# Kernel tuning notes

Measured on AMD Instinct MI355X. Metric: run time of the kernel, lower is better.

Reference implementation:

```python
import jax, jax.numpy as jnp
import numpy as np
import math

MAX2D = 1001        # max_2d_position_embeddings
COORD = 128         # coordinate_size
SHAPE = 128         # shape_size
PE = 384            # pos_embed_size
HID = 768           # layout_hidden_size
PAD = 0             # pad_token_id
EPS = 1e-12
INIT = 1024         # sinusoidal init_size
BIG = 100000000


def sinusoidal_table(num_embeddings=INIT, dim=PE, padding_idx=PAD):
    half = dim // 2
    freq = np.exp(np.arange(half, dtype=np.float32) * (-math.log(10000.0) / (half - 1)))
    ang = np.arange(num_embeddings, dtype=np.float32)[:, None] * freq[None, :]
    tab = np.concatenate([np.sin(ang), np.cos(ang)], axis=1)
    if padding_idx is not None:
        tab[padding_idx, :] = 0.0
    return jnp.asarray(tab, dtype=jnp.float32)


def setup_inputs() -> dict:
    key = jax.random.key(0)
    ks = jax.random.split(key, 16)
    B, L = 2, 1024
    x1 = jax.random.randint(ks[0], (B, L), 0, 501, dtype=jnp.int32)
    y1 = jax.random.randint(ks[1], (B, L), 0, 501, dtype=jnp.int32)
    w = jax.random.randint(ks[2], (B, L), 0, 500, dtype=jnp.int32)
    h = jax.random.randint(ks[3], (B, L), 0, 500, dtype=jnp.int32)
    bbox = jnp.stack([x1, y1, x1 + w, y1 + h], axis=-1)  # [B,L,4], 0..1000
    attention_mask = jnp.ones((B, L), dtype=jnp.int32)
    s = 0.02
    inp = {
        'bbox': bbox,
        'attention_mask': attention_mask,
        'x_tab': jax.random.normal(ks[4], (MAX2D, COORD), jnp.float32) * s,
        'y_tab': jax.random.normal(ks[5], (MAX2D, COORD), jnp.float32) * s,
        'h_tab': jax.random.normal(ks[6], (MAX2D, SHAPE), jnp.float32) * s,
        'w_tab': jax.random.normal(ks[7], (MAX2D, SHAPE), jnp.float32) * s,
        'W_tl_w': jax.random.normal(ks[8], (HID, 2 * PE), jnp.float32) * s,
        'W_tl_b': jnp.zeros((HID,), jnp.float32),
        'W_tr_w': jax.random.normal(ks[9], (HID, 2 * PE), jnp.float32) * s,
        'W_tr_b': jnp.zeros((HID,), jnp.float32),
        'W_bl_w': jax.random.normal(ks[10], (HID, 2 * PE), jnp.float32) * s,
        'W_bl_b': jnp.zeros((HID,), jnp.float32),
        'W_br_w': jax.random.normal(ks[11], (HID, 2 * PE), jnp.float32) * s,
        'W_br_b': jnp.zeros((HID,), jnp.float32),
        'ln_g': jnp.ones((HID,), jnp.float32),
        'ln_b': jnp.zeros((HID,), jnp.float32),
        'params': 50,
    }
    return inp


def _knn_graph(bbox, mask, topk):
    # mask out padded boxes with a huge coordinate (matches masked_fill)
    bm = jnp.where((mask == 0)[..., None], BIG, bbox).astype(jnp.float32)
    xc = (bm[:, :, 0] + bm[:, :, 2]) / 2.0
    yc = (bm[:, :, 1] + bm[:, :, 3]) / 2.0
    dist = (xc[:, :, None] - xc[:, None, :]) ** 2 + (yc[:, :, None] - yc[:, None, :]) ** 2
    _, topk_index = jax.lax.top_k(-dist, topk)  # smallest distances
    topk_index = topk_index.astype(jnp.int32)
    B, L, _ = topk_index.shape
    lm = jnp.zeros((B, L, L), jnp.int32)
    b_ix = jnp.arange(B)[:, None, None]
    l_ix = jnp.arange(L)[None, :, None]
    lm = lm.at[b_ix, l_ix, topk_index].set(1)
    return topk_index, lm


def _rel_pos_emb(bbox, topk_index, sin_tab):
    # diff[b,i,k] = coord[b,i] - coord[b,topk_index[b,i,k]]
    gather = jax.vmap(lambda v, idx: v[idx])  # per-batch gather

    def diffs(c):
        d = c[:, :, None] - gather(c, topk_index)
        d = jnp.clip(d, 1 - MAX2D, MAX2D - 1)
        # torch negative indexing into the table wraps: idx % INIT
        return sin_tab[jnp.mod(d, INIT)]  # [B,L,K,PE]

    ex1 = diffs(bbox[:, :, 0])
    ey1 = diffs(bbox[:, :, 1])
    ex2 = diffs(bbox[:, :, 2])
    ey2 = diffs(bbox[:, :, 3])
    return ex1, ey1, ex2, ey2


def _linear(x, w, b):
    return jnp.einsum('blki,oi->blko', x, w) + b


def reference(bbox, attention_mask, x_tab, y_tab, h_tab, w_tab,
              W_tl_w, W_tl_b, W_tr_w, W_tr_b, W_bl_w, W_bl_b, W_br_w, W_br_b,
              ln_g, ln_b, params):
    sin_tab = sinusoidal_table()
    # spatial position embeddings
    layout_emb = jnp.concatenate([
        x_tab[bbox[:, :, 0]], y_tab[bbox[:, :, 1]],
        x_tab[bbox[:, :, 2]], y_tab[bbox[:, :, 3]],
        h_tab[bbox[:, :, 3] - bbox[:, :, 1]],
        w_tab[bbox[:, :, 2] - bbox[:, :, 0]],
    ], axis=-1)  # [B,L,HID]

    topk = min(bbox.shape[1], int(params))
    topk_index, local_mask = _knn_graph(bbox, attention_mask, topk)

    ex1, ey1, ex2, ey2 = _rel_pos_emb(bbox, topk_index, sin_tab)
    p = (_linear(jnp.concatenate([ex1, ey1], -1), W_tl_w, W_tl_b)
         + _linear(jnp.concatenate([ex2, ey1], -1), W_tr_w, W_tr_b)
         + _linear(jnp.concatenate([ex1, ey2], -1), W_bl_w, W_bl_b)
         + _linear(jnp.concatenate([ex2, ey2], -1), W_br_w, W_br_b))

    mu = jnp.mean(layout_emb, axis=-1, keepdims=True)
    var = jnp.mean((layout_emb - mu) ** 2, axis=-1, keepdims=True)
    layout_emb = (layout_emb - mu) / jnp.sqrt(var + EPS) * ln_g + ln_b
    # dropout is identity in eval mode
    return layout_emb, p, topk_index, local_mask
```

## Files before the change

kernel.cpp:

```cpp
#include <hip/hip_runtime.h>
#include <math.h>

namespace {
constexpr int B_ = 2;
constexpr int L_ = 1024;
constexpr int K_ = 50;
constexpr int HID_ = 768;
constexpr int PE_ = 384;
constexpr int HALF_ = 192;
constexpr int TROWS_ = 1024;

constexpr long long OUT0 = 0;
constexpr long long OUT1 = OUT0 + (long long)B_ * L_ * HID_;
constexpr long long OUT2 = OUT1 + (long long)B_ * L_ * K_ * HID_;
constexpr long long OUT3 = OUT2 + (long long)B_ * L_ * K_;

constexpr long long WS_SIN = 0;
constexpr long long WS_T   = WS_SIN + (long long)TROWS_ * PE_;
constexpr long long WS_TI  = WS_T + 4LL * TROWS_ * HID_;
}

__global__ __launch_bounds__(192) void k_sin_tab(float* __restrict__ tab) {
    const int r = blockIdx.x;
    const int j = threadIdx.x;
    const float c = -0.04822168780092243f;
    float fr = expf((float)j * c);
    float ang = (float)r * fr;
    float s, co;
    if (r == 0) { s = 0.f; co = 0.f; } else { s = sinf(ang); co = cosf(ang); }
    tab[r * PE_ + j] = s;
    tab[r * PE_ + HALF_ + j] = co;
}

__global__ __launch_bounds__(256) void k_build_T(
    const float* __restrict__ sinT,
    const float* __restrict__ Wtl, const float* __restrict__ Wtr,
    const float* __restrict__ Wbl, const float* __restrict__ Wbr,
    const float* __restrict__ btl, const float* __restrict__ btr,
    const float* __restrict__ bbl, const float* __restrict__ bbr,
    float* __restrict__ Tout)
{
    const int t = blockIdx.z;
    const float* Wa; const float* Wb; int coff;
    if (t == 0)      { Wa = Wtl; Wb = Wbl; coff = 0; }
    else if (t == 1) { Wa = Wtr; Wb = Wbr; coff = 0; }
    else if (t == 2) { Wa = Wtl; Wb = Wtr; coff = PE_; }
    else             { Wa = Wbl; Wb = Wbr; coff = PE_; }

    __shared__ float As[32][65];
    __shared__ float Bs[32][65];
    const int tid = threadIdx.x;
    const int r0 = blockIdx.x * 64;
    const int o0 = blockIdx.y * 64;
    const int ty = tid >> 4, tx = tid & 15;
    float acc[4][4] = {{0.f, 0.f, 0.f, 0.f}, {0.f, 0.f, 0.f, 0.f},
                       {0.f, 0.f, 0.f, 0.f}, {0.f, 0.f, 0.f, 0.f}};

    for (int k0 = 0; k0 < PE_; k0 += 32) {
        #pragma unroll
        for (int s = 0; s < 8; ++s) {
            int l = s * 256 + tid;
            int rr = l >> 5, jj = l & 31;
            As[jj][rr] = sinT[(r0 + rr) * PE_ + k0 + jj];
            Bs[jj][rr] = Wa[(o0 + rr) * (2 * PE_) + coff + k0 + jj]
                       + Wb[(o0 + rr) * (2 * PE_) + coff + k0 + jj];
        }
        __syncthreads();
        #pragma unroll
        for (int kk = 0; kk < 32; ++kk) {
            float a[4], b[4];
            #pragma unroll
            for (int m = 0; m < 4; ++m) a[m] = As[kk][ty * 4 + m];
            #pragma unroll
            for (int n = 0; n < 4; ++n) b[n] = Bs[kk][tx * 4 + n];
            #pragma unroll
            for (int m = 0; m < 4; ++m)
                #pragma unroll
                for (int n = 0; n < 4; ++n)
                    acc[m][n] = fmaf(a[m], b[n], acc[m][n]);
        }
        __syncthreads();
    }

    #pragma unroll
    for (int m = 0; m < 4; ++m) {
        int r = r0 + ty * 4 + m;
        #pragma unroll
        for (int n = 0; n < 4; ++n) {
            int o = o0 + tx * 4 + n;
            float v = acc[m][n];
            if (t == 0) v += btl[o] + btr[o] + bbl[o] + bbr[o];
            Tout[(long long)t * TROWS_ * HID_ + (long long)r * HID_ + o] = v;
        }
    }
}

__device__ __forceinline__ float block_sum_256(float x, float* red) {
    #pragma unroll
    for (int off = 32; off > 0; off >>= 1) x += __shfl_xor(x, off, 64);
    const int wave = threadIdx.x >> 6;
    if ((threadIdx.x & 63) == 0) red[wave] = x;
    __syncthreads();
    float t = red[0] + red[1] + red[2] + red[3];
    __syncthreads();
    return t;
}

__global__ __launch_bounds__(256) void k_layout_emb(
    const int4* __restrict__ bbox, const float* __restrict__ xt,
    const float* __restrict__ yt, const float* __restrict__ ht,
    const float* __restrict__ wt, const float* __restrict__ g,
    const float* __restrict__ bb, float* __restrict__ out)
{
    __shared__ float red[4];
    const int tok = blockIdx.x;
    const int4 q = bbox[tok];
    const int tid = threadIdx.x;
    float v[3];
    #pragma unroll
    for (int s = 0; s < 3; ++s) {
        int e = tid + s * 256;
        int off = e & 127;
        int seg = e >> 7;
        float val;
        if (seg == 0)      val = xt[q.x * 128 + off];
        else if (seg == 1) val = yt[q.y * 128 + off];
        else if (seg == 2) val = xt[q.z * 128 + off];
        else if (seg == 3) val = yt[q.w * 128 + off];
        else if (seg == 4) val = ht[(q.w - q.y) * 128 + off];
        else               val = wt[(q.z - q.x) * 128 + off];
        v[s] = val;
    }
    float mu = block_sum_256(v[0] + v[1] + v[2], red) * (1.0f / 768.0f);
    float sq = 0.f;
    #pragma unroll
    for (int s = 0; s < 3; ++s) { float d = v[s] - mu; sq = fmaf(d, d, sq); }
    float var = block_sum_256(sq, red) * (1.0f / 768.0f);
    float inv = 1.0f / sqrtf(var + 1e-12f);
    float* orow = out + (long long)tok * HID_;
    #pragma unroll
    for (int s = 0; s < 3; ++s) {
        int e = tid + s * 256;
        orow[e] = (v[s] - mu) * inv * g[e] + bb[e];
    }
}

__global__ __launch_bounds__(256) void k_topk(
    const int4* __restrict__ bbox, const int* __restrict__ am,
    float* __restrict__ topk_f, int* __restrict__ topk_i,
    float* __restrict__ mask)
{
    __shared__ float xs[L_], ys[L_];
    __shared__ unsigned long long wmin[4];
    const int bx = blockIdx.x;
    const int b = bx >> 10;
    const int i = bx & 1023;
    const int tid = threadIdx.x;
    for (int j = tid; j < L_; j += 256) {
        int4 q = bbox[b * L_ + j];
        float x1, y1, x2, y2;
        if (am[b * L_ + j] == 0) { x1 = y1 = x2 = y2 = 1e8f; }
        else { x1 = (float)q.x; y1 = (float)q.y; x2 = (float)q.z; y2 = (float)q.w; }
        xs[j] = (x1 + x2) * 0.5f;
        ys[j] = (y1 + y2) * 0.5f;
    }
    __syncthreads();
    const float xq = xs[i], yq = ys[i];
    unsigned long long key[4];
    #pragma unroll
    for (int s = 0; s < 4; ++s) {
        int j = tid + s * 256;
        float dx = xq - xs[j], dy = yq - ys[j];
        float d = dx * dx + dy * dy;
        key[s] = ((unsigned long long)__float_as_uint(d) << 32) | (unsigned int)j;
    }
    const int lane = tid & 63, wave = tid >> 6;
    const long long obase = (long long)(b * L_ + i) * K_;
    float* mrow = mask + (long long)(b * L_ + i) * L_;
    for (int r = 0; r < K_; ++r) {
        unsigned long long m = key[0] < key[1] ? key[0] : key[1];
        unsigned long long m2 = key[2] < key[3] ? key[2] : key[3];
        if (m2 < m) m = m2;
        #pragma unroll
        for (int off = 1; off < 64; off <<= 1) {
            unsigned long long o = __shfl_xor(m, off, 64);
            if (o < m) m = o;
        }
        if (lane == 0) wmin[wave] = m;
        __syncthreads();
        unsigned long long mm = wmin[0] < wmin[1] ? wmin[0] : wmin[1];
        unsigned long long mb = wmin[2] < wmin[3] ? wmin[2] : wmin[3];
        if (mb < mm) mm = mb;
        if (tid == 0) {
            int w = (int)(mm & 0xffffffffu);
            topk_f[obase + r] = (float)w;
            topk_i[obase + r] = w;
            mrow[w] = 1.0f;
        }
        #pragma unroll
        for (int s = 0; s < 4; ++s) if (key[s] == mm) key[s] = ~0ULL;
        __syncthreads();
    }
}

__device__ __forceinline__ int wrapc(int d) {
    d = d < -1000 ? -1000 : (d > 1000 ? 1000 : d);
    return (d + 1024) & 1023;
}

__global__ __launch_bounds__(256) void k_passemble(
    const int4* __restrict__ bbox, const int* __restrict__ topk_i,
    const float4* __restrict__ T, float* __restrict__ p)
{
    const int row = blockIdx.x * 4 + (threadIdx.x >> 6);
    const int lane = threadIdx.x & 63;
    const int b = row / (L_ * K_);
    const int rem = row - b * (L_ * K_);
    const int i = rem / K_;
    const int j = topk_i[row];
    const int4 bi = bbox[b * L_ + i];
    const int4 bj = bbox[b * L_ + j];
    const float4* T1 = T + (long long)wrapc(bi.x - bj.x) * 192;
    const float4* T2 = T + 196608 + (long long)wrapc(bi.z - bj.z) * 192;
    const float4* T3 = T + 2 * 196608 + (long long)wrapc(bi.y - bj.y) * 192;
    const float4* T4 = T + 3 * 196608 + (long long)wrapc(bi.w - bj.w) * 192;
    float4* prow = (float4*)p + (long long)row * 192;
    #pragma unroll
    for (int u = 0; u < 3; ++u) {
        int f = lane + u * 64;
        float4 a = T1[f], c = T2[f], d = T3[f], e = T4[f];
        float4 o;
        o.x = a.x + c.x + d.x + e.x;
        o.y = a.y + c.y + d.y + e.y;
        o.z = a.z + c.z + d.z + e.z;
        o.w = a.w + c.w + d.w + e.w;
        prow[f] = o;
    }
}

extern "C" void kernel_launch(void* const* d_in, const int* in_sizes, int n_in,
                              void* d_out, int out_size, void* d_ws, size_t ws_size,
                              hipStream_t stream)
{
    const int4* bbox = (const int4*)d_in[0];
    const int* am    = (const int*)d_in[1];
    const float* xt  = (const float*)d_in[2];
    const float* yt  = (const float*)d_in[3];
    const float* ht  = (const float*)d_in[4];
    const float* wt  = (const float*)d_in[5];
    const float* Wtl = (const float*)d_in[6];
    const float* btl = (const float*)d_in[7];
    const float* Wtr = (const float*)d_in[8];
    const float* btr = (const float*)d_in[9];
    const float* Wbl = (const float*)d_in[10];
    const float* bbl = (const float*)d_in[11];
    const float* Wbr = (const float*)d_in[12];
    const float* bbr = (const float*)d_in[13];
    const float* lng = (const float*)d_in[14];
    const float* lnb = (const float*)d_in[15];

    float* out = (float*)d_out;
    float* ws = (float*)d_ws;
    float* sinT = ws + WS_SIN;
    float* T = ws + WS_T;
    int* topk_i = (int*)(ws + WS_TI);

    hipMemsetAsync(out + OUT3, 0, (size_t)B_ * L_ * L_ * sizeof(float), stream);

    k_sin_tab<<<dim3(TROWS_), dim3(HALF_), 0, stream>>>(sinT);
    k_build_T<<<dim3(16, 12, 4), dim3(256), 0, stream>>>(
        sinT, Wtl, Wtr, Wbl, Wbr, btl, btr, bbl, bbr, T);
    k_layout_emb<<<dim3(B_ * L_), dim3(256), 0, stream>>>(
        bbox, xt, yt, ht, wt, lng, lnb, out + OUT0);
    k_topk<<<dim3(B_ * L_), dim3(256), 0, stream>>>(
        bbox, am, out + OUT2, topk_i, out + OUT3);
    k_passemble<<<dim3(B_ * L_ * K_ / 4), dim3(256), 0, stream>>>(
        bbox, topk_i, (const float4*)T, out + OUT1);
}
```

Baseline: 559.2 us.

## Build local mask in LDS, drop memset, use nontemporal streaming stores

The top-k kernel now builds each row of the local mask in shared memory and writes the full row once with vectorized nontemporal stores. This removes the separate memset of the 8 MB mask and its scattered single-element global writes. The large p output and the layout embedding are also written with nontemporal stores to avoid polluting the cache on write-once data. Correctness depends on every mask row being fully written by its block, which holds because 256 threads each store one float4 covering 1024 entries.

```diff
diff --git a/kernel.cpp b/kernel.cpp
--- a/kernel.cpp
+++ b/kernel.cpp
@@ -9,6 +9,8 @@
 constexpr int PE_ = 384;
 constexpr int HALF_ = 192;
 constexpr int TROWS_ = 1024;
+
+typedef float f32x4 __attribute__((ext_vector_type(4)));
 
 constexpr long long OUT0 = 0;
 constexpr long long OUT1 = OUT0 + (long long)B_ * L_ * HID_;
@@ -141,7 +143,7 @@
     #pragma unroll
     for (int s = 0; s < 3; ++s) {
         int e = tid + s * 256;
-        orow[e] = (v[s] - mu) * inv * g[e] + bb[e];
+        __builtin_nontemporal_store((v[s] - mu) * inv * g[e] + bb[e], orow + e);
     }
 }
 
@@ -151,6 +153,7 @@
     float* __restrict__ mask)
 {
     __shared__ float xs[L_], ys[L_];
+    __shared__ float mrow_s[L_];
     __shared__ unsigned long long wmin[4];
     const int bx = blockIdx.x;
     const int b = bx >> 10;
@@ -163,6 +166,7 @@
         else { x1 = (float)q.x; y1 = (float)q.y; x2 = (float)q.z; y2 = (float)q.w; }
         xs[j] = (x1 + x2) * 0.5f;
         ys[j] = (y1 + y2) * 0.5f;
+        mrow_s[j] = 0.f;
     }
     __syncthreads();
     const float xq = xs[i], yq = ys[i];
@@ -176,7 +180,6 @@
     }
     const int lane = tid & 63, wave = tid >> 6;
     const long long obase = (long long)(b * L_ + i) * K_;
-    float* mrow = mask + (long long)(b * L_ + i) * L_;
     for (int r = 0; r < K_; ++r) {
         unsigned long long m = key[0] < key[1] ? key[0] : key[1];
         unsigned long long m2 = key[2] < key[3] ? key[2] : key[3];
@@ -195,12 +198,15 @@
             int w = (int)(mm & 0xffffffffu);
             topk_f[obase + r] = (float)w;
             topk_i[obase + r] = w;
-            mrow[w] = 1.0f;
+            mrow_s[w] = 1.0f;
         }
         #pragma unroll
         for (int s = 0; s < 4; ++s) if (key[s] == mm) key[s] = ~0ULL;
         __syncthreads();
     }
+    f32x4* mrow = (f32x4*)(mask + (long long)(b * L_ + i) * L_);
+    const f32x4* src = (const f32x4*)mrow_s;
+    __builtin_nontemporal_store(src[tid], mrow + tid);
 }
 
 __device__ __forceinline__ int wrapc(int d) {
@@ -210,7 +216,7 @@
 
 __global__ __launch_bounds__(256) void k_passemble(
     const int4* __restrict__ bbox, const int* __restrict__ topk_i,
-    const float4* __restrict__ T, float* __restrict__ p)
+    const f32x4* __restrict__ T, float* __restrict__ p)
 {
     const int row = blockIdx.x * 4 + (threadIdx.x >> 6);
     const int lane = threadIdx.x & 63;
@@ -220,21 +226,16 @@
     const int j = topk_i[row];
     const int4 bi = bbox[b * L_ + i];
     const int4 bj = bbox[b * L_ + j];
-    const float4* T1 = T + (long long)wrapc(bi.x - bj.x) * 192;
-    const float4* T2 = T + 196608 + (long long)wrapc(bi.z - bj.z) * 192;
-    const float4* T3 = T + 2 * 196608 + (long long)wrapc(bi.y - bj.y) * 192;
-    const float4* T4 = T + 3 * 196608 + (long long)wrapc(bi.w - bj.w) * 192;
-    float4* prow = (float4*)p + (long long)row * 192;
+    const f32x4* T1 = T + (long long)wrapc(bi.x - bj.x) * 192;
+    const f32x4* T2 = T + 196608 + (long long)wrapc(bi.z - bj.z) * 192;
+    const f32x4* T3 = T + 2 * 196608 + (long long)wrapc(bi.y - bj.y) * 192;
+    const f32x4* T4 = T + 3 * 196608 + (long long)wrapc(bi.w - bj.w) * 192;
+    f32x4* prow = (f32x4*)p + (long long)row * 192;
     #pragma unroll
     for (int u = 0; u < 3; ++u) {
         int f = lane + u * 64;
-        float4 a = T1[f], c = T2[f], d = T3[f], e = T4[f];
-        float4 o;
-        o.x = a.x + c.x + d.x + e.x;
-        o.y = a.y + c.y + d.y + e.y;
-        o.z = a.z + c.z + d.z + e.z;
-        o.w = a.w + c.w + d.w + e.w;
-        prow[f] = o;
+        f32x4 o = T1[f] + T2[f] + T3[f] + T4[f];
+        __builtin_nontemporal_store(o, prow + f);
     }
 }
 
@@ -265,8 +266,6 @@
     float* T = ws + WS_T;
     int* topk_i = (int*)(ws + WS_TI);
 
-    hipMemsetAsync(out + OUT3, 0, (size_t)B_ * L_ * L_ * sizeof(float), stream);
-
     k_sin_tab<<<dim3(TROWS_), dim3(HALF_), 0, stream>>>(sinT);
     k_build_T<<<dim3(16, 12, 4), dim3(256), 0, stream>>>(
         sinT, Wtl, Wtr, Wbl, Wbr, btl, btr, bbl, bbr, T);
@@ -275,5 +274,5 @@
     k_topk<<<dim3(B_ * L_), dim3(256), 0, stream>>>(
         bbox, am, out + OUT2, topk_i, out + OUT3);
     k_passemble<<<dim3(B_ * L_ * K_ / 4), dim3(256), 0, stream>>>(
-        bbox, topk_i, (const float4*)T, out + OUT1);
-}
+        bbox, topk_i, (const f32x4*)T, out + OUT1);
+}
```

Result: faster. 522.0 us (-6.6%).
